# Kernel optimization log

Measured on AMD Instinct MI355X. Metric: run time of the kernel, lower is better.

## Reference

```python
import jax, jax.numpy as jnp
import numpy as np

B, T, E, S, W, H = 2, 2048, 256, 128, 8, 150

def _mlp(x, w1, b1, w2, b2, w3, b3):
    # Score module: Linear->ReLU->Linear->ReLU->Linear (dropout inactive in eval)
    h = jax.nn.relu(x @ w1 + b1)
    h = jax.nn.relu(h @ w2 + b2)
    return h @ w3 + b3

def _mlp_params(key, d_in):
    k1, k2, k3 = jax.random.split(key, 3)
    s = 0.02
    return (s * jax.random.normal(k1, (d_in, H), jnp.float32), jnp.zeros((H,), jnp.float32),
            s * jax.random.normal(k2, (H, H), jnp.float32), jnp.zeros((H,), jnp.float32),
            s * jax.random.normal(k3, (H, 1), jnp.float32), jnp.zeros((1,), jnp.float32))

def setup_inputs() -> dict:
    key = jax.random.key(0)
    ke, ks, ka, km, kp = jax.random.split(key, 5)
    inp = {
        'batch_embeds': jax.random.normal(ke, (B, T, E), jnp.float32),
        'span_starts': jax.random.randint(ks, (B, S), 0, T - W, jnp.int32),
    }
    for name, k, d in [('attn', ka, E), ('ment', km, 3 * E), ('pair', kp, 9 * E)]:
        w1, b1, w2, b2, w3, b3 = _mlp_params(k, d)
        inp.update({f'{name}_w1': w1, f'{name}_b1': b1, f'{name}_w2': w2,
                    f'{name}_b2': b2, f'{name}_w3': w3, f'{name}_b3': b3})
    return inp

def reference(batch_embeds, span_starts,
              attn_w1, attn_b1, attn_w2, attn_b2, attn_w3, attn_b3,
              ment_w1, ment_b1, ment_w2, ment_b2, ment_w3, ment_b3,
              pair_w1, pair_b1, pair_w2, pair_b2, pair_w3, pair_b3):
    # ---- MentionScore ----
    attns = _mlp(batch_embeds, attn_w1, attn_b1, attn_w2, attn_b2, attn_w3, attn_b3)  # [B,T,1]
    spans = span_starts[:, :, None] + jnp.arange(W)                                   # [B,S,W]
    flat = spans.reshape(B, S * W)
    emb_spans = jnp.take_along_axis(batch_embeds, flat[:, :, None], axis=1).reshape(B, S, W, E)
    attn_spans = jnp.take_along_axis(attns, flat[:, :, None], axis=1).reshape(B, S, W, 1)
    start = emb_spans[:, :, 0, :]
    end = emb_spans[:, :, -1, :]
    weighted = jnp.sum(emb_spans * attn_spans, axis=2)                                # [B,S,E]
    g_i = jnp.concatenate([start, end, weighted], axis=-1)                            # [B,S,3E]
    mention_scores = _mlp(g_i, ment_w1, ment_b1, ment_w2, ment_b2, ment_w3, ment_b3)  # [B,S,1]
    # ---- PairwiseScore: all-pairs cat(g_i, g_j, g_i*g_j) ----
    gi = jnp.broadcast_to(g_i[:, :, None, :], (B, S, S, 3 * E))
    gj = jnp.broadcast_to(g_i[:, None, :, :], (B, S, S, 3 * E))
    pairs = jnp.concatenate([gi, gj, gi * gj], axis=-1)                               # [B,S,S,9E]
    pair_scores = _mlp(pairs, pair_w1, pair_b1, pair_w2, pair_b2, pair_w3, pair_b3)   # [B,S,S,1]
    # extended score = mean(mention_i, mention_j, pair_ij)
    ext = (mention_scores[:, :, None, :] + mention_scores[:, None, :, :] + pair_scores) / 3.0
    return ext
```

## Files before the change

### kernel.cpp

```cpp
#include <hip/hip_runtime.h>
#include <hip/hip_bf16.h>


typedef __bf16 bf16;
typedef __attribute__((ext_vector_type(8))) short v8s;
typedef __attribute__((ext_vector_type(8))) __bf16 v8bf;
typedef __attribute__((ext_vector_type(4))) float v4f;

#define MFMA_BF16(A, B, C) __builtin_amdgcn_mfma_f32_16x16x32_bf16((A), (B), (C), 0, 0, 0)

__device__ __forceinline__ v8bf mul_cvt8(float4 xa, float4 xb, float4 sa, float4 sb) {
    v8bf w;
    w[0] = (bf16)(xa.x * sa.x); w[1] = (bf16)(xa.y * sa.y);
    w[2] = (bf16)(xa.z * sa.z); w[3] = (bf16)(xa.w * sa.w);
    w[4] = (bf16)(xb.x * sb.x); w[5] = (bf16)(xb.y * sb.y);
    w[6] = (bf16)(xb.z * sb.z); w[7] = (bf16)(xb.w * sb.w);
    return w;
}
__device__ __forceinline__ v8bf cvt8(float4 xa, float4 xb) {
    v8bf w;
    w[0] = (bf16)xa.x; w[1] = (bf16)xa.y; w[2] = (bf16)xa.z; w[3] = (bf16)xa.w;
    w[4] = (bf16)xb.x; w[5] = (bf16)xb.y; w[6] = (bf16)xb.z; w[7] = (bf16)xb.w;
    return w;
}

__global__ __launch_bounds__(256) void prep_kernel(
    const float* __restrict__ pw1, const float* __restrict__ pw2,
    const float* __restrict__ aw1, const float* __restrict__ aw2,
    const float* __restrict__ mw1, const float* __restrict__ mw2,
    const float* __restrict__ pb1, const float* __restrict__ pb2, const float* __restrict__ pw3,
    const float* __restrict__ ab1, const float* __restrict__ ab2, const float* __restrict__ aw3,
    const float* __restrict__ mb1, const float* __restrict__ mb2, const float* __restrict__ mw3,
    bf16* __restrict__ w1cT, bf16* __restrict__ w2pT,
    bf16* __restrict__ w1aT, bf16* __restrict__ w2aT, bf16* __restrict__ w2mT,
    bf16* __restrict__ wuvmT, float* __restrict__ bias)
{
    int idx = blockIdx.x * 256 + threadIdx.x;
    if (idx < 147456) {
        int h = idx / 768, e = idx % 768;
        w1cT[idx] = (bf16)((h < 150) ? pw1[(1536 + e) * 150 + h] : 0.f);
    } else if (idx < 178176) {
        int j = idx - 147456; int n = j / 160, k = j % 160;
        w2pT[j] = (bf16)((n < 150 && k < 150) ? pw2[k * 150 + n] : 0.f);
    } else if (idx < 227328) {
        int j = idx - 178176; int h = j / 256, e = j % 256;
        w1aT[j] = (bf16)((h < 150) ? aw1[e * 150 + h] : 0.f);
    } else if (idx < 258048) {
        int j = idx - 227328; int n = j / 160, k = j % 160;
        w2aT[j] = (bf16)((n < 150 && k < 150) ? aw2[k * 150 + n] : 0.f);
    } else if (idx < 288768) {
        int j = idx - 258048; int n = j / 160, k = j % 160;
        w2mT[j] = (bf16)((n < 150 && k < 150) ? mw2[k * 150 + n] : 0.f);
    } else if (idx < 731136) {
        int j = idx - 288768; int s = j / 147456; int r = j % 147456;
        int h = r / 768, e = r % 768;
        float v = 0.f;
        if (h < 150) {
            if (s == 0)      v = pw1[e * 150 + h];
            else if (s == 1) v = pw1[(768 + e) * 150 + h];
            else             v = mw1[e * 150 + h];
        }
        wuvmT[j] = (bf16)v;
    } else if (idx < 732864) {
        int j = idx - 731136; int arr = j / 192, h = j % 192;
        const float* src;
        switch (arr) {
            case 0: src = pb1; break; case 1: src = pb2; break; case 2: src = pw3; break;
            case 3: src = ab1; break; case 4: src = ab2; break; case 5: src = aw3; break;
            case 6: src = mb1; break; case 7: src = mb2; break; default: src = mw3; break;
        }
        bias[j] = (h < 150) ? src[h] : 0.f;
    }
}

__global__ __launch_bounds__(256) void build_g_kernel(
    const float* __restrict__ emb, const int* __restrict__ spans,
    const float* __restrict__ attns, float* __restrict__ g)
{
    int blk = blockIdx.x;
    int b = blk >> 7;
    int t0 = spans[blk];
    int e = threadIdx.x;
    const float* eb = emb + ((size_t)(b * 2048 + t0)) * 256 + e;
    const float* at = attns + b * 2048 + t0;
    float start = eb[0];
    float endv  = eb[7 * 256];
    float wsum = 0.f;
#pragma unroll
    for (int w = 0; w < 8; ++w) wsum = fmaf(eb[w * 256], at[w], wsum);
    g[(size_t)blk * 768 + e]       = start;
    g[(size_t)blk * 768 + 256 + e] = endv;
    g[(size_t)blk * 768 + 512 + e] = wsum;
}

#define A32_ELEMS 2304
#define A64_ELEMS 4608
#define B_ELEMS   13824

__global__ __launch_bounds__(512, 4) void attn_mfma_kernel(
    const float* __restrict__ emb,
    const bf16* __restrict__ w1aT, const bf16* __restrict__ w2aT,
    const float* __restrict__ b1p, const float* __restrict__ b2p,
    const float* __restrict__ w3p, const float* __restrict__ b3,
    float* __restrict__ attns)
{
    __shared__ __attribute__((aligned(16))) char smem[64512];
    bf16*  a_lds  = (bf16*)smem;
    bf16*  b_lds  = (bf16*)(smem + 9216);
    bf16*  h1_lds = (bf16*)smem;
    float* red    = (float*)(smem + 10752);

    const int m0  = blockIdx.x * 32;
    const int tid = threadIdx.x;
    const int lane = tid & 63;
    const int wm = (tid >> 6) >> 2, wn = (tid >> 6) & 3;
    const int l15 = lane & 15, lk = (lane >> 4) * 8;
    const int aj = tid >> 3, ae = (tid & 7) * 8;
    const int br = tid >> 3, bc = (tid & 7) * 8;
    const float* gA = emb + (size_t)(m0 + (aj & 31)) * 256 + ae;

    {
        if (tid < 256) {
            float4 x0 = *(const float4*)(gA + 0), x1 = *(const float4*)(gA + 4);
            *(v8bf*)(a_lds + aj * 72 + ae) = cvt8(x0, x1);
        }
#pragma unroll
        for (int s2 = 0; s2 < 3; ++s2) {
            const int row = br + s2 * 64;
            *(uint4*)(b_lds + row * 72 + bc) = *(const uint4*)(w1aT + row * 256 + bc);
        }
    }
    __syncthreads();

    v4f acc[3];
#pragma unroll
    for (int nf = 0; nf < 3; ++nf) acc[nf] = (v4f){0.f, 0.f, 0.f, 0.f};

    for (int c = 0; c < 4; ++c) {
        float4 x0, x1;
        uint4 b0, b1, b2;
        if (c < 3) {
            const int e0 = (c + 1) * 64;
            if (tid < 256) { x0 = *(const float4*)(gA + e0); x1 = *(const float4*)(gA + e0 + 4); }
            b0 = *(const uint4*)(w1aT + (br +   0) * 256 + e0 + bc);
            b1 = *(const uint4*)(w1aT + (br +  64) * 256 + e0 + bc);
            b2 = *(const uint4*)(w1aT + (br + 128) * 256 + e0 + bc);
        }
        const bf16* ab = a_lds + (c & 1) * A32_ELEMS;
        const bf16* bb = b_lds + (c & 1) * B_ELEMS;
#pragma unroll
        for (int ks = 0; ks < 2; ++ks) {
            const int kb = ks * 32 + lk;
            v8s af = *(const v8s*)&ab[(wm * 16 + l15) * 72 + kb];
            v8s bfr[3];
#pragma unroll
            for (int nf = 0; nf < 3; ++nf)
                bfr[nf] = *(const v8s*)&bb[(wn * 48 + nf * 16 + l15) * 72 + kb];
#pragma unroll
            for (int nf = 0; nf < 3; ++nf)
                acc[nf] = MFMA_BF16(af, bfr[nf], acc[nf]);
        }
        if (c < 3) {
            bf16* bdst = b_lds + ((c + 1) & 1) * B_ELEMS;
            if (tid < 256)
                *(v8bf*)(a_lds + ((c + 1) & 1) * A32_ELEMS + aj * 72 + ae) = cvt8(x0, x1);
            *(uint4*)(bdst + (br +   0) * 72 + bc) = b0;
            *(uint4*)(bdst + (br +  64) * 72 + bc) = b1;
            *(uint4*)(bdst + (br + 128) * 72 + bc) = b2;
        }
        __syncthreads();
    }

    {
        const float b10 = b1p[wn * 48 + 0  + l15];
        const float b11 = b1p[wn * 48 + 16 + l15];
        const float b12 = b1p[wn * 48 + 32 + l15];
#pragma unroll
        for (int r = 0; r < 4; ++r) {
            const int jl = wm * 16 + (lane >> 4) * 4 + r;
            bf16* hrow = h1_lds + jl * 168 + wn * 48 + l15;
            hrow[0] = (bf16)fmaxf(acc[0][r] + b10, 0.f);
            if (wn < 3) {
                hrow[16] = (bf16)fmaxf(acc[1][r] + b11, 0.f);
                hrow[32] = (bf16)fmaxf(acc[2][r] + b12, 0.f);
            }
        }
    }
    __syncthreads();

    v4f acc2[3];
#pragma unroll
    for (int nf = 0; nf < 3; ++nf) acc2[nf] = (v4f){0.f, 0.f, 0.f, 0.f};
#pragma unroll
    for (int ks = 0; ks < 5; ++ks) {
        const int kb = ks * 32 + lk;
        v8s af = *(const v8s*)&h1_lds[(wm * 16 + l15) * 168 + kb];
        v8s bfr[3];
#pragma unroll
        for (int nf = 0; nf < 3; ++nf)
            bfr[nf] = *(const v8s*)&w2aT[(size_t)(wn * 48 + nf * 16 + l15) * 160 + kb];
#pragma unroll
        for (int nf = 0; nf < 3; ++nf)
            acc2[nf] = MFMA_BF16(af, bfr[nf], acc2[nf]);
    }

    const float b2v0 = b2p[wn * 48 + 0  + l15], w3v0 = w3p[wn * 48 + 0  + l15];
    const float b2v1 = b2p[wn * 48 + 16 + l15], w3v1 = w3p[wn * 48 + 16 + l15];
    const float b2v2 = b2p[wn * 48 + 32 + l15], w3v2 = w3p[wn * 48 + 32 + l15];
#pragma unroll
    for (int r = 0; r < 4; ++r) {
        float p = fmaxf(acc2[0][r] + b2v0, 0.f) * w3v0
                + fmaxf(acc2[1][r] + b2v1, 0.f) * w3v1
                + fmaxf(acc2[2][r] + b2v2, 0.f) * w3v2;
        p += __shfl_xor(p, 1);
        p += __shfl_xor(p, 2);
        p += __shfl_xor(p, 4);
        p += __shfl_xor(p, 8);
        if (l15 == 0) {
            const int jl = wm * 16 + (lane >> 4) * 4 + r;
            red[jl * 4 + wn] = p;
        }
    }
    __syncthreads();
    if (tid < 32) {
        attns[m0 + tid] = red[tid * 4 + 0] + red[tid * 4 + 1]
                        + red[tid * 4 + 2] + red[tid * 4 + 3] + b3[0];
    }
}

__global__ __launch_bounds__(512, 4) void uvm_mfma_kernel(
    const float* __restrict__ g, const bf16* __restrict__ wuvmT,
    const bf16* __restrict__ w2mT,
    const float* __restrict__ pb1p, const float* __restrict__ mb1p,
    const float* __restrict__ mb2p, const float* __restrict__ mw3p,
    const float* __restrict__ mb3,
    float* __restrict__ u_pad, float* __restrict__ v_pad, float* __restrict__ ment)
{
    __shared__ __attribute__((aligned(16))) char smem[64512];
    bf16*  a_lds  = (bf16*)smem;
    bf16*  b_lds  = (bf16*)(smem + 9216);
    bf16*  h1_lds = (bf16*)smem;
    float* red    = (float*)(smem + 10752);

    const int sect = blockIdx.x >> 3;
    const int m0   = (blockIdx.x & 7) * 32;
    const bf16* Bw = wuvmT + (size_t)sect * 147456;
    const int tid = threadIdx.x;
    const int lane = tid & 63;
    const int wm = (tid >> 6) >> 2, wn = (tid >> 6) & 3;
    const int l15 = lane & 15, lk = (lane >> 4) * 8;
    const int aj = tid >> 3, ae = (tid & 7) * 8;
    const int br = tid >> 3, bc = (tid & 7) * 8;
    const float* gA = g + (size_t)(m0 + (aj & 31)) * 768 + ae;

    {
        if (tid < 256) {
            float4 x0 = *(const float4*)(gA + 0), x1 = *(const float4*)(gA + 4);
            *(v8bf*)(a_lds + aj * 72 + ae) = cvt8(x0, x1);
        }
#pragma unroll
        for (int s2 = 0; s2 < 3; ++s2) {
            const int row = br + s2 * 64;
            *(uint4*)(b_lds + row * 72 + bc) = *(const uint4*)(Bw + row * 768 + bc);
        }
    }
    __syncthreads();

    v4f acc[3];
#pragma unroll
    for (int nf = 0; nf < 3; ++nf) acc[nf] = (v4f){0.f, 0.f, 0.f, 0.f};

    for (int c = 0; c < 12; ++c) {
        float4 x0, x1;
        uint4 b0, b1, b2;
        if (c < 11) {
            const int e0 = (c + 1) * 64;
            if (tid < 256) { x0 = *(const float4*)(gA + e0); x1 = *(const float4*)(gA + e0 + 4); }
            b0 = *(const uint4*)(Bw + (br +   0) * 768 + e0 + bc);
            b1 = *(const uint4*)(Bw + (br +  64) * 768 + e0 + bc);
            b2 = *(const uint4*)(Bw + (br + 128) * 768 + e0 + bc);
        }
        const bf16* ab = a_lds + (c & 1) * A32_ELEMS;
        const bf16* bb = b_lds + (c & 1) * B_ELEMS;
#pragma unroll
        for (int ks = 0; ks < 2; ++ks) {
            const int kb = ks * 32 + lk;
            v8s af = *(const v8s*)&ab[(wm * 16 + l15) * 72 + kb];
            v8s bfr[3];
#pragma unroll
            for (int nf = 0; nf < 3; ++nf)
                bfr[nf] = *(const v8s*)&bb[(wn * 48 + nf * 16 + l15) * 72 + kb];
#pragma unroll
            for (int nf = 0; nf < 3; ++nf)
                acc[nf] = MFMA_BF16(af, bfr[nf], acc[nf]);
        }
        if (c < 11) {
            bf16* bdst = b_lds + ((c + 1) & 1) * B_ELEMS;
            if (tid < 256)
                *(v8bf*)(a_lds + ((c + 1) & 1) * A32_ELEMS + aj * 72 + ae) = cvt8(x0, x1);
            *(uint4*)(bdst + (br +   0) * 72 + bc) = b0;
            *(uint4*)(bdst + (br +  64) * 72 + bc) = b1;
            *(uint4*)(bdst + (br + 128) * 72 + bc) = b2;
        }
        __syncthreads();
    }

    if (sect < 2) {
        float* dst = (sect == 0) ? u_pad : v_pad;
        const float bb0 = (sect == 0) ? pb1p[wn * 48 + 0  + l15] : 0.f;
        const float bb1 = (sect == 0) ? pb1p[wn * 48 + 16 + l15] : 0.f;
        const float bb2 = (sect == 0) ? pb1p[wn * 48 + 32 + l15] : 0.f;
#pragma unroll
        for (int r = 0; r < 4; ++r) {
            const int jl = wm * 16 + (lane >> 4) * 4 + r;
            float* drow = dst + (size_t)(m0 + jl) * 192 + wn * 48 + l15;
            drow[0]  = acc[0][r] + bb0;
            drow[16] = acc[1][r] + bb1;
            drow[32] = acc[2][r] + bb2;
        }
        return;
    }

    {
        const float b10 = mb1p[wn * 48 + 0  + l15];
        const float b11 = mb1p[wn * 48 + 16 + l15];
        const float b12 = mb1p[wn * 48 + 32 + l15];
#pragma unroll
        for (int r = 0; r < 4; ++r) {
            const int jl = wm * 16 + (lane >> 4) * 4 + r;
            bf16* hrow = h1_lds + jl * 168 + wn * 48 + l15;
            hrow[0] = (bf16)fmaxf(acc[0][r] + b10, 0.f);
            if (wn < 3) {
                hrow[16] = (bf16)fmaxf(acc[1][r] + b11, 0.f);
                hrow[32] = (bf16)fmaxf(acc[2][r] + b12, 0.f);
            }
        }
    }
    __syncthreads();

    v4f acc2[3];
#pragma unroll
    for (int nf = 0; nf < 3; ++nf) acc2[nf] = (v4f){0.f, 0.f, 0.f, 0.f};
#pragma unroll
    for (int ks = 0; ks < 5; ++ks) {
        const int kb = ks * 32 + lk;
        v8s af = *(const v8s*)&h1_lds[(wm * 16 + l15) * 168 + kb];
        v8s bfr[3];
#pragma unroll
        for (int nf = 0; nf < 3; ++nf)
            bfr[nf] = *(const v8s*)&w2mT[(size_t)(wn * 48 + nf * 16 + l15) * 160 + kb];
#pragma unroll
        for (int nf = 0; nf < 3; ++nf)
            acc2[nf] = MFMA_BF16(af, bfr[nf], acc2[nf]);
    }

    const float b2v0 = mb2p[wn * 48 + 0  + l15], w3v0 = mw3p[wn * 48 + 0  + l15];
    const float b2v1 = mb2p[wn * 48 + 16 + l15], w3v1 = mw3p[wn * 48 + 16 + l15];
    const float b2v2 = mb2p[wn * 48 + 32 + l15], w3v2 = mw3p[wn * 48 + 32 + l15];
#pragma unroll
    for (int r = 0; r < 4; ++r) {
        float p = fmaxf(acc2[0][r] + b2v0, 0.f) * w3v0
                + fmaxf(acc2[1][r] + b2v1, 0.f) * w3v1
                + fmaxf(acc2[2][r] + b2v2, 0.f) * w3v2;
        p += __shfl_xor(p, 1);
        p += __shfl_xor(p, 2);
        p += __shfl_xor(p, 4);
        p += __shfl_xor(p, 8);
        if (l15 == 0) {
            const int jl = wm * 16 + (lane >> 4) * 4 + r;
            red[jl * 4 + wn] = p;
        }
    }
    __syncthreads();
    if (tid < 32) {
        ment[m0 + tid] = red[tid * 4 + 0] + red[tid * 4 + 1]
                       + red[tid * 4 + 2] + red[tid * 4 + 3] + mb3[0];
    }
}

__global__ __launch_bounds__(512, 4) void pair_mfma_kernel(
    const float* __restrict__ g,
    const float* __restrict__ u_pad, const float* __restrict__ v_pad,
    const bf16* __restrict__ w1cT, const bf16* __restrict__ w2T,
    const float* __restrict__ b2_pad, const float* __restrict__ w3_pad,
    const float* __restrict__ pb3, const float* __restrict__ ment,
    float* __restrict__ out)
{
    __shared__ __attribute__((aligned(16))) char smem[76800];
    bf16*  a_lds  = (bf16*)smem;
    bf16*  b_lds  = (bf16*)(smem + 18432);
    float* gi_s   = (float*)(smem + 73728);
    bf16*  h1_lds = (bf16*)smem;
    float* red    = (float*)(smem + 22528);

    const int blk = blockIdx.x;
    const int b = blk >> 8;
    const int i = (blk >> 1) & 127;
    const int half = blk & 1;
    const int row_i = b * 128 + i;
    const int jg0 = b * 128 + half * 64;
    const int tid = threadIdx.x;
    const int lane = tid & 63;
    const int wm = (tid >> 6) >> 2, wn = (tid >> 6) & 3;
    const int l15 = lane & 15, lk = (lane >> 4) * 8;
    const int aj = tid >> 3, ae = (tid & 7) * 8;
    const int br = tid >> 3, bc = (tid & 7) * 8;
    const float* gA = g + (size_t)(jg0 + aj) * 768 + ae;

    if (tid < 192)
        *(float4*)&gi_s[tid * 4] = *(const float4*)&g[(size_t)row_i * 768 + tid * 4];
    __syncthreads();

    {
        float4 x0 = *(const float4*)(gA + 0), x1 = *(const float4*)(gA + 4);
        const float* gp = gi_s + ae;
        float4 s0 = *(const float4*)(gp + 0), s1 = *(const float4*)(gp + 4);
        *(v8bf*)(a_lds + aj * 72 + ae) = mul_cvt8(x0, x1, s0, s1);
#pragma unroll
        for (int s2 = 0; s2 < 3; ++s2) {
            const int row = br + s2 * 64;
            *(uint4*)(b_lds + row * 72 + bc) = *(const uint4*)(w1cT + row * 768 + bc);
        }
    }
    __syncthreads();

    v4f acc[2][3];
#pragma unroll
    for (int mf = 0; mf < 2; ++mf)
#pragma unroll
        for (int nf = 0; nf < 3; ++nf) acc[mf][nf] = (v4f){0.f, 0.f, 0.f, 0.f};

    for (int c = 0; c < 12; ++c) {
        float4 x0, x1;
        uint4 b0, b1, b2;
        if (c < 11) {
            const int e0 = (c + 1) * 64;
            x0 = *(const float4*)(gA + e0);
            x1 = *(const float4*)(gA + e0 + 4);
            b0 = *(const uint4*)(w1cT + (br +   0) * 768 + e0 + bc);
            b1 = *(const uint4*)(w1cT + (br +  64) * 768 + e0 + bc);
            b2 = *(const uint4*)(w1cT + (br + 128) * 768 + e0 + bc);
        }
        const bf16* ab = a_lds + (c & 1) * A64_ELEMS;
        const bf16* bb = b_lds + (c & 1) * B_ELEMS;
#pragma unroll
        for (int ks = 0; ks < 2; ++ks) {
            const int kb = ks * 32 + lk;
            v8s af[2], bfr[3];
#pragma unroll
            for (int mf = 0; mf < 2; ++mf)
                af[mf] = *(const v8s*)&ab[(wm * 32 + mf * 16 + l15) * 72 + kb];
#pragma unroll
            for (int nf = 0; nf < 3; ++nf)
                bfr[nf] = *(const v8s*)&bb[(wn * 48 + nf * 16 + l15) * 72 + kb];
#pragma unroll
            for (int mf = 0; mf < 2; ++mf)
#pragma unroll
                for (int nf = 0; nf < 3; ++nf)
                    acc[mf][nf] = MFMA_BF16(af[mf], bfr[nf], acc[mf][nf]);
        }
        if (c < 11) {
            const float* gp = gi_s + (c + 1) * 64 + ae;
            float4 s0 = *(const float4*)(gp + 0), s1 = *(const float4*)(gp + 4);
            bf16* bdst = b_lds + ((c + 1) & 1) * B_ELEMS;
            *(v8bf*)(a_lds + ((c + 1) & 1) * A64_ELEMS + aj * 72 + ae) =
                mul_cvt8(x0, x1, s0, s1);
            *(uint4*)(bdst + (br +   0) * 72 + bc) = b0;
            *(uint4*)(bdst + (br +  64) * 72 + bc) = b1;
            *(uint4*)(bdst + (br + 128) * 72 + bc) = b2;
        }
        __syncthreads();
    }

    {
        const float uh0 = u_pad[row_i * 192 + wn * 48 + 0  + l15];
        const float uh1 = u_pad[row_i * 192 + wn * 48 + 16 + l15];
        const float uh2 = u_pad[row_i * 192 + wn * 48 + 32 + l15];
#pragma unroll
        for (int mf = 0; mf < 2; ++mf) {
#pragma unroll
            for (int r = 0; r < 4; ++r) {
                const int jl = wm * 32 + mf * 16 + (lane >> 4) * 4 + r;
                const float* vrow = v_pad + (size_t)(jg0 + jl) * 192 + wn * 48 + l15;
                const float v0 = acc[mf][0][r] + uh0 + vrow[0];
                const float v1 = acc[mf][1][r] + uh1 + vrow[16];
                const float v2 = acc[mf][2][r] + uh2 + vrow[32];
                bf16* hrow = h1_lds + jl * 168 + wn * 48 + l15;
                hrow[0] = (bf16)fmaxf(v0, 0.f);
                if (wn < 3) {
                    hrow[16] = (bf16)fmaxf(v1, 0.f);
                    hrow[32] = (bf16)fmaxf(v2, 0.f);
                }
            }
        }
    }
    __syncthreads();

    v4f acc2[2][3];
#pragma unroll
    for (int mf = 0; mf < 2; ++mf)
#pragma unroll
        for (int nf = 0; nf < 3; ++nf) acc2[mf][nf] = (v4f){0.f, 0.f, 0.f, 0.f};
#pragma unroll
    for (int ks = 0; ks < 5; ++ks) {
        const int kb = ks * 32 + lk;
        v8s af[2], bfr[3];
#pragma unroll
        for (int mf = 0; mf < 2; ++mf)
            af[mf] = *(const v8s*)&h1_lds[(wm * 32 + mf * 16 + l15) * 168 + kb];
#pragma unroll
        for (int nf = 0; nf < 3; ++nf)
            bfr[nf] = *(const v8s*)&w2T[(size_t)(wn * 48 + nf * 16 + l15) * 160 + kb];
#pragma unroll
        for (int mf = 0; mf < 2; ++mf)
#pragma unroll
            for (int nf = 0; nf < 3; ++nf)
                acc2[mf][nf] = MFMA_BF16(af[mf], bfr[nf], acc2[mf][nf]);
    }

    const float b2v0 = b2_pad[wn * 48 + 0  + l15], w3v0 = w3_pad[wn * 48 + 0  + l15];
    const float b2v1 = b2_pad[wn * 48 + 16 + l15], w3v1 = w3_pad[wn * 48 + 16 + l15];
    const float b2v2 = b2_pad[wn * 48 + 32 + l15], w3v2 = w3_pad[wn * 48 + 32 + l15];
#pragma unroll
    for (int mf = 0; mf < 2; ++mf) {
#pragma unroll
        for (int r = 0; r < 4; ++r) {
            float p = fmaxf(acc2[mf][0][r] + b2v0, 0.f) * w3v0
                    + fmaxf(acc2[mf][1][r] + b2v1, 0.f) * w3v1
                    + fmaxf(acc2[mf][2][r] + b2v2, 0.f) * w3v2;
            p += __shfl_xor(p, 1);
            p += __shfl_xor(p, 2);
            p += __shfl_xor(p, 4);
            p += __shfl_xor(p, 8);
            if (l15 == 0) {
                const int jl = wm * 32 + mf * 16 + (lane >> 4) * 4 + r;
                red[jl * 4 + wn] = p;
            }
        }
    }
    __syncthreads();
    if (tid < 64) {
        const float s = red[tid * 4 + 0] + red[tid * 4 + 1] + red[tid * 4 + 2] + red[tid * 4 + 3];
        out[(size_t)b * 16384 + (size_t)i * 128 + half * 64 + tid] =
            (s + pb3[0] + ment[row_i] + ment[b * 128 + half * 64 + tid]) * (1.f / 3.f);
    }
}

extern "C" void kernel_launch(void* const* d_in, const int* in_sizes, int n_in,
                              void* d_out, int out_size, void* d_ws, size_t ws_size,
                              hipStream_t stream)
{
    const float* emb   = (const float*)d_in[0];
    const int*   spans = (const int*)d_in[1];
    const float* aw1 = (const float*)d_in[2];
    const float* ab1 = (const float*)d_in[3];
    const float* aw2 = (const float*)d_in[4];
    const float* ab2 = (const float*)d_in[5];
    const float* aw3 = (const float*)d_in[6];
    const float* ab3 = (const float*)d_in[7];
    const float* mw1 = (const float*)d_in[8];
    const float* mb1 = (const float*)d_in[9];
    const float* mw2 = (const float*)d_in[10];
    const float* mb2 = (const float*)d_in[11];
    const float* mw3 = (const float*)d_in[12];
    const float* mb3 = (const float*)d_in[13];
    const float* pw1 = (const float*)d_in[14];
    const float* pb1 = (const float*)d_in[15];
    const float* pw2 = (const float*)d_in[16];
    const float* pb2 = (const float*)d_in[17];
    const float* pw3 = (const float*)d_in[18];
    const float* pb3 = (const float*)d_in[19];

    float* ws    = (float*)d_ws;
    float* attns = ws;
    float* g     = ws + 4096;
    float* ment  = ws + 200704;
    float* u_pad = ws + 200960;
    float* v_pad = ws + 250112;
    float* bias  = ws + 299264;
    float* pb1p = bias;         float* pb2p = bias + 192;  float* pw3p = bias + 384;
    float* ab1p = bias + 576;   float* ab2p = bias + 768;  float* aw3p = bias + 960;
    float* mb1p = bias + 1152;  float* mb2p = bias + 1344; float* mw3p = bias + 1536;
    bf16* w1cT  = (bf16*)(ws + 300992);
    bf16* w2pT  = (bf16*)(ws + 374720);
    bf16* w1aT  = (bf16*)(ws + 390080);
    bf16* w2aT  = (bf16*)(ws + 414656);
    bf16* w2mT  = (bf16*)(ws + 430016);
    bf16* wuvmT = (bf16*)(ws + 445376);

    prep_kernel<<<2863, 256, 0, stream>>>(pw1, pw2, aw1, aw2, mw1, mw2,
                                          pb1, pb2, pw3, ab1, ab2, aw3, mb1, mb2, mw3,
                                          w1cT, w2pT, w1aT, w2aT, w2mT, wuvmT, bias);
    attn_mfma_kernel<<<128, 512, 0, stream>>>(emb, w1aT, w2aT, ab1p, ab2p, aw3p, ab3, attns);
    build_g_kernel<<<256, 256, 0, stream>>>(emb, spans, attns, g);
    uvm_mfma_kernel<<<24, 512, 0, stream>>>(g, wuvmT, w2mT, pb1p, mb1p, mb2p, mw3p, mb3,
                                            u_pad, v_pad, ment);
    pair_mfma_kernel<<<512, 512, 0, stream>>>(g, u_pad, v_pad, w1cT, w2pT,
                                              pb2p, pw3p, pb3, ment, (float*)d_out);
}
```

Measured before the change: 62.68 us.

## Deepen global prefetch to two chunks ahead in the three GEMM K-loops

Measured after the change: 57.67 us (median of 2 runs). 8.0% less time.

```diff
diff --git a/kernel.cpp b/kernel.cpp
--- a/kernel.cpp
+++ b/kernel.cpp
@@ -119,6 +119,25 @@
     const int br = tid >> 3, bc = (tid & 7) * 8;
     const float* gA = emb + (size_t)(m0 + (aj & 31)) * 256 + ae;
 
+    v4f acc[3];
+#pragma unroll
+    for (int nf = 0; nf < 3; ++nf) acc[nf] = (v4f){0.f, 0.f, 0.f, 0.f};
+
+#define ATTN_COMPUTE(AB, BB)                                                   \
+    do {                                                                       \
+        _Pragma("unroll")                                                      \
+        for (int ks = 0; ks < 2; ++ks) {                                       \
+            const int kb = ks * 32 + lk;                                       \
+            v8s af = *(const v8s*)&(AB)[(wm * 16 + l15) * 72 + kb];            \
+            v8s bf0 = *(const v8s*)&(BB)[(wn * 48 +  0 + l15) * 72 + kb];      \
+            v8s bf1 = *(const v8s*)&(BB)[(wn * 48 + 16 + l15) * 72 + kb];      \
+            v8s bf2 = *(const v8s*)&(BB)[(wn * 48 + 32 + l15) * 72 + kb];      \
+            acc[0] = MFMA_BF16(af, bf0, acc[0]);                               \
+            acc[1] = MFMA_BF16(af, bf1, acc[1]);                               \
+            acc[2] = MFMA_BF16(af, bf2, acc[2]);                               \
+        }                                                                      \
+    } while (0)
+
     {
         if (tid < 256) {
             float4 x0 = *(const float4*)(gA + 0), x1 = *(const float4*)(gA + 4);
@@ -130,43 +149,44 @@
             *(uint4*)(b_lds + row * 72 + bc) = *(const uint4*)(w1aT + row * 256 + bc);
         }
     }
-    __syncthreads();
-
-    v4f acc[3];
-#pragma unroll
-    for (int nf = 0; nf < 3; ++nf) acc[nf] = (v4f){0.f, 0.f, 0.f, 0.f};
-
-    for (int c = 0; c < 4; ++c) {
-        float4 x0, x1;
-        uint4 b0, b1, b2;
-        if (c < 3) {
-            const int e0 = (c + 1) * 64;
-            if (tid < 256) { x0 = *(const float4*)(gA + e0); x1 = *(const float4*)(gA + e0 + 4); }
-            b0 = *(const uint4*)(w1aT + (br +   0) * 256 + e0 + bc);
-            b1 = *(const uint4*)(w1aT + (br +  64) * 256 + e0 + bc);
-            b2 = *(const uint4*)(w1aT + (br + 128) * 256 + e0 + bc);
-        }
-        const bf16* ab = a_lds + (c & 1) * A32_ELEMS;
-        const bf16* bb = b_lds + (c & 1) * B_ELEMS;
-#pragma unroll
-        for (int ks = 0; ks < 2; ++ks) {
-            const int kb = ks * 32 + lk;
-            v8s af = *(const v8s*)&ab[(wm * 16 + l15) * 72 + kb];
-            v8s bfr[3];
-#pragma unroll
-            for (int nf = 0; nf < 3; ++nf)
-                bfr[nf] = *(const v8s*)&bb[(wn * 48 + nf * 16 + l15) * 72 + kb];
-#pragma unroll
-            for (int nf = 0; nf < 3; ++nf)
-                acc[nf] = MFMA_BF16(af, bfr[nf], acc[nf]);
-        }
-        if (c < 3) {
-            bf16* bdst = b_lds + ((c + 1) & 1) * B_ELEMS;
+    float4 xB0, xB1; uint4 bB0, bB1, bB2;
+    if (tid < 256) { xB0 = *(const float4*)(gA + 64); xB1 = *(const float4*)(gA + 68); }
+    bB0 = *(const uint4*)(w1aT + (br +   0) * 256 + 64 + bc);
+    bB1 = *(const uint4*)(w1aT + (br +  64) * 256 + 64 + bc);
+    bB2 = *(const uint4*)(w1aT + (br + 128) * 256 + 64 + bc);
+    __syncthreads();
+
+    float4 xA0, xA1; uint4 bA0, bA1, bA2;
+    for (int cc = 0; cc < 2; ++cc) {
+        const int c = cc * 2;
+        if (cc < 1) {
+            const int e0 = (c + 2) * 64;
+            if (tid < 256) { xA0 = *(const float4*)(gA + e0); xA1 = *(const float4*)(gA + e0 + 4); }
+            bA0 = *(const uint4*)(w1aT + (br +   0) * 256 + e0 + bc);
+            bA1 = *(const uint4*)(w1aT + (br +  64) * 256 + e0 + bc);
+            bA2 = *(const uint4*)(w1aT + (br + 128) * 256 + e0 + bc);
+        }
+        ATTN_COMPUTE(a_lds, b_lds);
+        if (tid < 256)
+            *(v8bf*)(a_lds + A32_ELEMS + aj * 72 + ae) = cvt8(xB0, xB1);
+        *(uint4*)(b_lds + B_ELEMS + (br +   0) * 72 + bc) = bB0;
+        *(uint4*)(b_lds + B_ELEMS + (br +  64) * 72 + bc) = bB1;
+        *(uint4*)(b_lds + B_ELEMS + (br + 128) * 72 + bc) = bB2;
+        __syncthreads();
+        if (cc < 1) {
+            const int e0 = (c + 3) * 64;
+            if (tid < 256) { xB0 = *(const float4*)(gA + e0); xB1 = *(const float4*)(gA + e0 + 4); }
+            bB0 = *(const uint4*)(w1aT + (br +   0) * 256 + e0 + bc);
+            bB1 = *(const uint4*)(w1aT + (br +  64) * 256 + e0 + bc);
+            bB2 = *(const uint4*)(w1aT + (br + 128) * 256 + e0 + bc);
+        }
+        ATTN_COMPUTE(a_lds + A32_ELEMS, b_lds + B_ELEMS);
+        if (cc < 1) {
             if (tid < 256)
-                *(v8bf*)(a_lds + ((c + 1) & 1) * A32_ELEMS + aj * 72 + ae) = cvt8(x0, x1);
-            *(uint4*)(bdst + (br +   0) * 72 + bc) = b0;
-            *(uint4*)(bdst + (br +  64) * 72 + bc) = b1;
-            *(uint4*)(bdst + (br + 128) * 72 + bc) = b2;
+                *(v8bf*)(a_lds + aj * 72 + ae) = cvt8(xA0, xA1);
+            *(uint4*)(b_lds + (br +   0) * 72 + bc) = bA0;
+            *(uint4*)(b_lds + (br +  64) * 72 + bc) = bA1;
+            *(uint4*)(b_lds + (br + 128) * 72 + bc) = bA2;
         }
         __syncthreads();
     }
@@ -253,6 +273,10 @@
     const int br = tid >> 3, bc = (tid & 7) * 8;
     const float* gA = g + (size_t)(m0 + (aj & 31)) * 768 + ae;
 
+    v4f acc[3];
+#pragma unroll
+    for (int nf = 0; nf < 3; ++nf) acc[nf] = (v4f){0.f, 0.f, 0.f, 0.f};
+
     {
         if (tid < 256) {
             float4 x0 = *(const float4*)(gA + 0), x1 = *(const float4*)(gA + 4);
@@ -264,43 +288,44 @@
             *(uint4*)(b_lds + row * 72 + bc) = *(const uint4*)(Bw + row * 768 + bc);
         }
     }
-    __syncthreads();
-
-    v4f acc[3];
-#pragma unroll
-    for (int nf = 0; nf < 3; ++nf) acc[nf] = (v4f){0.f, 0.f, 0.f, 0.f};
-
-    for (int c = 0; c < 12; ++c) {
-        float4 x0, x1;
-        uint4 b0, b1, b2;
-        if (c < 11) {
-            const int e0 = (c + 1) * 64;
-            if (tid < 256) { x0 = *(const float4*)(gA + e0); x1 = *(const float4*)(gA + e0 + 4); }
-            b0 = *(const uint4*)(Bw + (br +   0) * 768 + e0 + bc);
-            b1 = *(const uint4*)(Bw + (br +  64) * 768 + e0 + bc);
-            b2 = *(const uint4*)(Bw + (br + 128) * 768 + e0 + bc);
-        }
-        const bf16* ab = a_lds + (c & 1) * A32_ELEMS;
-        const bf16* bb = b_lds + (c & 1) * B_ELEMS;
-#pragma unroll
-        for (int ks = 0; ks < 2; ++ks) {
-            const int kb = ks * 32 + lk;
-            v8s af = *(const v8s*)&ab[(wm * 16 + l15) * 72 + kb];
-            v8s bfr[3];
-#pragma unroll
-            for (int nf = 0; nf < 3; ++nf)
-                bfr[nf] = *(const v8s*)&bb[(wn * 48 + nf * 16 + l15) * 72 + kb];
-#pragma unroll
-            for (int nf = 0; nf < 3; ++nf)
-                acc[nf] = MFMA_BF16(af, bfr[nf], acc[nf]);
-        }
-        if (c < 11) {
-            bf16* bdst = b_lds + ((c + 1) & 1) * B_ELEMS;
+    float4 xB0, xB1; uint4 bB0, bB1, bB2;
+    if (tid < 256) { xB0 = *(const float4*)(gA + 64); xB1 = *(const float4*)(gA + 68); }
+    bB0 = *(const uint4*)(Bw + (br +   0) * 768 + 64 + bc);
+    bB1 = *(const uint4*)(Bw + (br +  64) * 768 + 64 + bc);
+    bB2 = *(const uint4*)(Bw + (br + 128) * 768 + 64 + bc);
+    __syncthreads();
+
+    float4 xA0, xA1; uint4 bA0, bA1, bA2;
+    for (int cc = 0; cc < 6; ++cc) {
+        const int c = cc * 2;
+        if (cc < 5) {
+            const int e0 = (c + 2) * 64;
+            if (tid < 256) { xA0 = *(const float4*)(gA + e0); xA1 = *(const float4*)(gA + e0 + 4); }
+            bA0 = *(const uint4*)(Bw + (br +   0) * 768 + e0 + bc);
+            bA1 = *(const uint4*)(Bw + (br +  64) * 768 + e0 + bc);
+            bA2 = *(const uint4*)(Bw + (br + 128) * 768 + e0 + bc);
+        }
+        ATTN_COMPUTE(a_lds, b_lds);
+        if (tid < 256)
+            *(v8bf*)(a_lds + A32_ELEMS + aj * 72 + ae) = cvt8(xB0, xB1);
+        *(uint4*)(b_lds + B_ELEMS + (br +   0) * 72 + bc) = bB0;
+        *(uint4*)(b_lds + B_ELEMS + (br +  64) * 72 + bc) = bB1;
+        *(uint4*)(b_lds + B_ELEMS + (br + 128) * 72 + bc) = bB2;
+        __syncthreads();
+        if (cc < 5) {
+            const int e0 = (c + 3) * 64;
+            if (tid < 256) { xB0 = *(const float4*)(gA + e0); xB1 = *(const float4*)(gA + e0 + 4); }
+            bB0 = *(const uint4*)(Bw + (br +   0) * 768 + e0 + bc);
+            bB1 = *(const uint4*)(Bw + (br +  64) * 768 + e0 + bc);
+            bB2 = *(const uint4*)(Bw + (br + 128) * 768 + e0 + bc);
+        }
+        ATTN_COMPUTE(a_lds + A32_ELEMS, b_lds + B_ELEMS);
+        if (cc < 5) {
             if (tid < 256)
-                *(v8bf*)(a_lds + ((c + 1) & 1) * A32_ELEMS + aj * 72 + ae) = cvt8(x0, x1);
-            *(uint4*)(bdst + (br +   0) * 72 + bc) = b0;
-            *(uint4*)(bdst + (br +  64) * 72 + bc) = b1;
-            *(uint4*)(bdst + (br + 128) * 72 + bc) = b2;
+                *(v8bf*)(a_lds + aj * 72 + ae) = cvt8(xA0, xA1);
+            *(uint4*)(b_lds + (br +   0) * 72 + bc) = bA0;
+            *(uint4*)(b_lds + (br +  64) * 72 + bc) = bA1;
+            *(uint4*)(b_lds + (br + 128) * 72 + bc) = bA2;
         }
         __syncthreads();
     }
@@ -411,6 +436,31 @@
         *(float4*)&gi_s[tid * 4] = *(const float4*)&g[(size_t)row_i * 768 + tid * 4];
     __syncthreads();
 
+    v4f acc[2][3];
+#pragma unroll
+    for (int mf = 0; mf < 2; ++mf)
+#pragma unroll
+        for (int nf = 0; nf < 3; ++nf) acc[mf][nf] = (v4f){0.f, 0.f, 0.f, 0.f};
+
+#define PAIR_COMPUTE(AB, BB)                                                   \
+    do {                                                                       \
+        _Pragma("unroll")                                                      \
+        for (int ks = 0; ks < 2; ++ks) {                                       \
+            const int kb = ks * 32 + lk;                                       \
+            v8s af0 = *(const v8s*)&(AB)[(wm * 32 +  0 + l15) * 72 + kb];      \
+            v8s af1 = *(const v8s*)&(AB)[(wm * 32 + 16 + l15) * 72 + kb];      \
+            v8s bf0 = *(const v8s*)&(BB)[(wn * 48 +  0 + l15) * 72 + kb];      \
+            v8s bf1 = *(const v8s*)&(BB)[(wn * 48 + 16 + l15) * 72 + kb];      \
+            v8s bf2 = *(const v8s*)&(BB)[(wn * 48 + 32 + l15) * 72 + kb];      \
+            acc[0][0] = MFMA_BF16(af0, bf0, acc[0][0]);                        \
+            acc[0][1] = MFMA_BF16(af0, bf1, acc[0][1]);                        \
+            acc[0][2] = MFMA_BF16(af0, bf2, acc[0][2]);                        \
+            acc[1][0] = MFMA_BF16(af1, bf0, acc[1][0]);                        \
+            acc[1][1] = MFMA_BF16(af1, bf1, acc[1][1]);                        \
+            acc[1][2] = MFMA_BF16(af1, bf2, acc[1][2]);                        \
+        }                                                                      \
+    } while (0)
+
     {
         float4 x0 = *(const float4*)(gA + 0), x1 = *(const float4*)(gA + 4);
         const float* gp = gi_s + ae;
@@ -422,52 +472,51 @@
             *(uint4*)(b_lds + row * 72 + bc) = *(const uint4*)(w1cT + row * 768 + bc);
         }
     }
-    __syncthreads();
-
-    v4f acc[2][3];
-#pragma unroll
-    for (int mf = 0; mf < 2; ++mf)
-#pragma unroll
-        for (int nf = 0; nf < 3; ++nf) acc[mf][nf] = (v4f){0.f, 0.f, 0.f, 0.f};
-
-    for (int c = 0; c < 12; ++c) {
-        float4 x0, x1;
-        uint4 b0, b1, b2;
-        if (c < 11) {
-            const int e0 = (c + 1) * 64;
-            x0 = *(const float4*)(gA + e0);
-            x1 = *(const float4*)(gA + e0 + 4);
-            b0 = *(const uint4*)(w1cT + (br +   0) * 768 + e0 + bc);
-            b1 = *(const uint4*)(w1cT + (br +  64) * 768 + e0 + bc);
-            b2 = *(const uint4*)(w1cT + (br + 128) * 768 + e0 + bc);
-        }
-        const bf16* ab = a_lds + (c & 1) * A64_ELEMS;
-        const bf16* bb = b_lds + (c & 1) * B_ELEMS;
-#pragma unroll
-        for (int ks = 0; ks < 2; ++ks) {
-            const int kb = ks * 32 + lk;
-            v8s af[2], bfr[3];
-#pragma unroll
-            for (int mf = 0; mf < 2; ++mf)
-                af[mf] = *(const v8s*)&ab[(wm * 32 + mf * 16 + l15) * 72 + kb];
-#pragma unroll
-            for (int nf = 0; nf < 3; ++nf)
-                bfr[nf] = *(const v8s*)&bb[(wn * 48 + nf * 16 + l15) * 72 + kb];
-#pragma unroll
-            for (int mf = 0; mf < 2; ++mf)
-#pragma unroll
-                for (int nf = 0; nf < 3; ++nf)
-                    acc[mf][nf] = MFMA_BF16(af[mf], bfr[nf], acc[mf][nf]);
-        }
-        if (c < 11) {
+    float4 xB0, xB1; uint4 bB0, bB1, bB2;
+    xB0 = *(const float4*)(gA + 64);
+    xB1 = *(const float4*)(gA + 68);
+    bB0 = *(const uint4*)(w1cT + (br +   0) * 768 + 64 + bc);
+    bB1 = *(const uint4*)(w1cT + (br +  64) * 768 + 64 + bc);
+    bB2 = *(const uint4*)(w1cT + (br + 128) * 768 + 64 + bc);
+    __syncthreads();
+
+    float4 xA0, xA1; uint4 bA0, bA1, bA2;
+    for (int cc = 0; cc < 6; ++cc) {
+        const int c = cc * 2;
+        if (cc < 5) {
+            const int e0 = (c + 2) * 64;
+            xA0 = *(const float4*)(gA + e0);
+            xA1 = *(const float4*)(gA + e0 + 4);
+            bA0 = *(const uint4*)(w1cT + (br +   0) * 768 + e0 + bc);
+            bA1 = *(const uint4*)(w1cT + (br +  64) * 768 + e0 + bc);
+            bA2 = *(const uint4*)(w1cT + (br + 128) * 768 + e0 + bc);
+        }
+        PAIR_COMPUTE(a_lds, b_lds);
+        {
             const float* gp = gi_s + (c + 1) * 64 + ae;
             float4 s0 = *(const float4*)(gp + 0), s1 = *(const float4*)(gp + 4);
-            bf16* bdst = b_lds + ((c + 1) & 1) * B_ELEMS;
-            *(v8bf*)(a_lds + ((c + 1) & 1) * A64_ELEMS + aj * 72 + ae) =
-                mul_cvt8(x0, x1, s0, s1);
-            *(uint4*)(bdst + (br +   0) * 72 + bc) = b0;
-            *(uint4*)(bdst + (br +  64) * 72 + bc) = b1;
-            *(uint4*)(bdst + (br + 128) * 72 + bc) = b2;
+            *(v8bf*)(a_lds + A64_ELEMS + aj * 72 + ae) = mul_cvt8(xB0, xB1, s0, s1);
+            *(uint4*)(b_lds + B_ELEMS + (br +   0) * 72 + bc) = bB0;
+            *(uint4*)(b_lds + B_ELEMS + (br +  64) * 72 + bc) = bB1;
+            *(uint4*)(b_lds + B_ELEMS + (br + 128) * 72 + bc) = bB2;
+        }
+        __syncthreads();
+        if (cc < 5) {
+            const int e0 = (c + 3) * 64;
+            xB0 = *(const float4*)(gA + e0);
+            xB1 = *(const float4*)(gA + e0 + 4);
+            bB0 = *(const uint4*)(w1cT + (br +   0) * 768 + e0 + bc);
+            bB1 = *(const uint4*)(w1cT + (br +  64) * 768 + e0 + bc);
+            bB2 = *(const uint4*)(w1cT + (br + 128) * 768 + e0 + bc);
+        }
+        PAIR_COMPUTE(a_lds + A64_ELEMS, b_lds + B_ELEMS);
+        if (cc < 5) {
+            const float* gp = gi_s + (c + 2) * 64 + ae;
+            float4 s0 = *(const float4*)(gp + 0), s1 = *(const float4*)(gp + 4);
+            *(v8bf*)(a_lds + aj * 72 + ae) = mul_cvt8(xA0, xA1, s0, s1);
+            *(uint4*)(b_lds + (br +   0) * 72 + bc) = bA0;
+            *(uint4*)(b_lds + (br +  64) * 72 + bc) = bA1;
+            *(uint4*)(b_lds + (br + 128) * 72 + bc) = bA2;
         }
         __syncthreads();
     }
```
